# Performance work log

Hardware: AMD Instinct MI355X
Metric: run time of the kernel (lower is better)

## Reference

```python
import jax, jax.numpy as jnp
import numpy as np

B, N, F_IN = 512, 128, 133
NHID, NHEADS, HID = 64, 8, 512
FP_DIM, FP2, TASKS = 1489, 512, 12
ALPHA = 0.2
NEG_BIG = -9e15


def _lin_init(key, fan_in, fan_out):
    return jax.random.normal(key, (fan_in, fan_out), jnp.float32) / np.sqrt(fan_in)


def setup_inputs() -> dict:
    key = jax.random.key(0)
    ks = jax.random.split(key, 24)
    inp = {
        'h': jax.random.normal(ks[0], (B, N, F_IN), jnp.float32),
        'adj': jax.random.randint(ks[1], (B, N, N), 0, 2, jnp.int32),
        'edge_feat': jax.random.uniform(ks[2], (B, N, N), jnp.float32),
        'fp': jax.random.uniform(ks[3], (B, FP_DIM), jnp.float32),
        # multi-head GAT layer params (a split as [a1; a2; a_edge])
        'W_heads': jax.random.normal(ks[4], (NHEADS, F_IN, NHID), jnp.float32) / np.sqrt(F_IN),
        'a1_heads': jax.random.normal(ks[5], (NHEADS, NHID), jnp.float32) / np.sqrt(NHID),
        'a2_heads': jax.random.normal(ks[6], (NHEADS, NHID), jnp.float32) / np.sqrt(NHID),
        'ae_heads': jax.random.normal(ks[7], (NHEADS,), jnp.float32) * 0.1,
        # output GAT layer
        'W_out': jax.random.normal(ks[8], (NHID * NHEADS, HID), jnp.float32) / np.sqrt(NHID * NHEADS),
        'a1_out': jax.random.normal(ks[9], (HID,), jnp.float32) / np.sqrt(HID),
        'a2_out': jax.random.normal(ks[10], (HID,), jnp.float32) / np.sqrt(HID),
        'ae_out': jax.random.normal(ks[11], ()) * 0.1,
        # FPN
        'fc1_w': _lin_init(ks[12], FP_DIM, FP2), 'fc1_b': jnp.zeros((FP2,), jnp.float32),
        'fc2_w': _lin_init(ks[13], FP2, HID), 'fc2_b': jnp.zeros((HID,), jnp.float32),
        # cross-attention fusion
        'q_w': _lin_init(ks[14], HID, HID), 'q_b': jnp.zeros((HID,), jnp.float32),
        'k_w': _lin_init(ks[15], HID, HID), 'k_b': jnp.zeros((HID,), jnp.float32),
        'v_w': _lin_init(ks[16], HID, HID), 'v_b': jnp.zeros((HID,), jnp.float32),
        'o_w': _lin_init(ks[17], HID, HID), 'o_b': jnp.zeros((HID,), jnp.float32),
        # FFN head
        'ffn1_w': _lin_init(ks[18], HID, HID), 'ffn1_b': jnp.zeros((HID,), jnp.float32),
        'ffn2_w': _lin_init(ks[19], HID, TASKS), 'ffn2_b': jnp.zeros((TASKS,), jnp.float32),
    }
    return inp


def _leaky(x):
    return jnp.where(x >= 0, x, ALPHA * x)


def _fpgnn_forward(h, adj, edge_feat, fp,
                   W_heads, a1_heads, a2_heads, ae_heads,
                   W_out, a1_out, a2_out, ae_out,
                   fc1_w, fc1_b, fc2_w, fc2_b,
                   q_w, q_b, k_w, k_b, v_w, v_b, o_w, o_b,
                   ffn1_w, ffn1_b, ffn2_w, ffn2_b):
    mask = adj > 0  # [B,N,N]
    # --- multi-head GAT layers (concat=True) ---
    Wh = jnp.einsum('bnf,hfd->bhnd', h, W_heads)            # [B,H,N,D]
    s1 = jnp.einsum('bhnd,hd->bhn', Wh, a1_heads)
    s2 = jnp.einsum('bhnd,hd->bhn', Wh, a2_heads)
    # e[b,h,i,j] = leaky(Wh_i.a1 + Wh_j.a2 + edge_ij*ae)  (exact decomposition of
    # the original concat([Wh_i, Wh_j, edge_ij]) @ a)
    e = _leaky(s1[:, :, :, None] + s2[:, :, None, :]
               + edge_feat[:, None, :, :] * ae_heads[None, :, None, None])
    att = jnp.where(mask[:, None], e, NEG_BIG)
    att = jax.nn.softmax(att, axis=-1)                       # softmax over dim=1 of [N,N]
    hp = jnp.einsum('bhij,bhjd->bhid', att, Wh)
    x = jax.nn.elu(hp)                                       # concat=True -> ELU
    x = jnp.transpose(x, (0, 2, 1, 3)).reshape(B, N, NHEADS * NHID)
    # --- output GAT layer (concat=False) ---
    Wx = x @ W_out                                           # [B,N,HID]
    t1 = Wx @ a1_out                                         # [B,N]
    t2 = Wx @ a2_out
    e2 = _leaky(t1[:, :, None] + t2[:, None, :] + edge_feat * ae_out)
    att2 = jnp.where(mask, e2, NEG_BIG)
    att2 = jax.nn.softmax(att2, axis=-1)
    hp2 = jnp.einsum('bij,bjd->bid', att2, Wx)
    gat_nodes = jax.nn.elu(hp2)                              # F.elu in GATOne
    gat_out = gat_nodes.mean(axis=1)                         # molecule readout [B,HID]
    # --- FPN ---
    fpn_out = jax.nn.relu(fp @ fc1_w + fc1_b) @ fc2_w + fc2_b  # [B,HID]
    # --- cross-attention fusion ---
    q = gat_out @ q_w + q_b
    k = fpn_out @ k_w + k_b
    v = fpn_out @ v_w + v_b
    score = jnp.sum(q * k, axis=-1, keepdims=True) / np.sqrt(HID)  # [B,1]
    weight = jax.nn.softmax(score[:, :, None], axis=-1)[:, :, 0]    # softmax over size-1 dim -> ones
    fused = q + weight * v
    fused = jax.nn.relu(fused @ o_w + o_b)
    # --- FFN head (dropout p=0, eval) ---
    out = jax.nn.relu(fused @ ffn1_w + ffn1_b) @ ffn2_w + ffn2_b
    return out


def reference(h, adj, edge_feat, fp,
              W_heads, a1_heads, a2_heads, ae_heads,
              W_out, a1_out, a2_out, ae_out,
              fc1_w, fc1_b, fc2_w, fc2_b,
              q_w, q_b, k_w, k_b, v_w, v_b, o_w, o_b,
              ffn1_w, ffn1_b, ffn2_w, ffn2_b):
    return _fpgnn_forward(h, adj, edge_feat, fp,
                          W_heads, a1_heads, a2_heads, ae_heads,
                          W_out, a1_out, a2_out, ae_out,
                          fc1_w, fc1_b, fc2_w, fc2_b,
                          q_w, q_b, k_w, k_b, v_w, v_b, o_w, o_b,
                          ffn1_w, ffn1_b, ffn2_w, ffn2_b)
```

## Files before the change

### kernel.cpp

```cpp
#include <hip/hip_runtime.h>
#include <hip/hip_bf16.h>


#define ALPHA_LK 0.2f
#define KP1 192
#define KPF 1536
#define MINF_BF16 0xFF80u

typedef unsigned short ushort_t;
typedef __attribute__((ext_vector_type(8))) short bfrag;
typedef __attribute__((ext_vector_type(4))) float ffrag;

__device__ __forceinline__ float b2f(ushort_t u) {
  return __uint_as_float(((unsigned)u) << 16);
}
__device__ __forceinline__ ushort_t f2b(float f) {
  unsigned u = __float_as_uint(f);
  unsigned r = (u + 0x7fffu + ((u >> 16) & 1u)) >> 16;
  return (ushort_t)r;
}
__device__ __forceinline__ float elu1(float v) {
  return v > 0.f ? v : __expf(v) - 1.f;
}
__device__ __forceinline__ void unpack8(uint4 u, ushort_t* e) {
  e[0] = u.x & 0xffff; e[1] = u.x >> 16;
  e[2] = u.y & 0xffff; e[3] = u.y >> 16;
  e[4] = u.z & 0xffff; e[5] = u.z >> 16;
  e[6] = u.w & 0xffff; e[7] = u.w >> 16;
}
__device__ __forceinline__ uint4 pack8(const ushort_t* o) {
  uint4 u;
  u.x = o[0] | ((unsigned)o[1] << 16);
  u.y = o[2] | ((unsigned)o[3] << 16);
  u.z = o[4] | ((unsigned)o[5] << 16);
  u.w = o[6] | ((unsigned)o[7] << 16);
  return u;
}

__device__ __forceinline__ void gll16(const void* g, void* l) {
  __builtin_amdgcn_global_load_lds(
      (const __attribute__((address_space(1))) unsigned int*)(unsigned long long)g,
      (__attribute__((address_space(3))) unsigned int*)(unsigned long long)l,
      16, 0, 0);
}

__global__ __launch_bounds__(256) void repack_h(const float* __restrict__ h,
                                                ushort_t* __restrict__ hb) {
  int o = blockIdx.x * 256 + threadIdx.x;
  int row = o / 48, c4 = (o - row * 48) * 4;
  const float* hr = h + (size_t)row * 133;
  ushort4 v;
  v.x = (c4 + 0 < 133) ? f2b(hr[c4 + 0]) : (ushort_t)0;
  v.y = (c4 + 1 < 133) ? f2b(hr[c4 + 1]) : (ushort_t)0;
  v.z = (c4 + 2 < 133) ? f2b(hr[c4 + 2]) : (ushort_t)0;
  v.w = (c4 + 3 < 133) ? f2b(hr[c4 + 3]) : (ushort_t)0;
  *(ushort4*)&hb[(size_t)row * KP1 + c4] = v;
}

__global__ __launch_bounds__(256) void repack_fp(const float* __restrict__ fp,
                                                 ushort_t* __restrict__ fpb) {
  int o = blockIdx.x * 256 + threadIdx.x;
  int row = o / 384, c4 = (o - row * 384) * 4;
  const float* fr = fp + (size_t)row * 1489;
  ushort4 v;
  v.x = (c4 + 0 < 1489) ? f2b(fr[c4 + 0]) : (ushort_t)0;
  v.y = (c4 + 1 < 1489) ? f2b(fr[c4 + 1]) : (ushort_t)0;
  v.z = (c4 + 2 < 1489) ? f2b(fr[c4 + 2]) : (ushort_t)0;
  v.w = (c4 + 3 < 1489) ? f2b(fr[c4 + 3]) : (ushort_t)0;
  *(ushort4*)&fpb[(size_t)row * KPF + c4] = v;
}

__global__ __launch_bounds__(256) void repack_w2t(const float* __restrict__ Whd,
                                                  ushort_t* __restrict__ W2t) {
  int o = blockIdx.x * 256 + threadIdx.x;
  if (o >= 512 * 48) return;
  int col = o / 48, c4 = (o - col * 48) * 4;
  int hh = col >> 6, d = col & 63;
  ushort4 v;
  v.x = (c4 + 0 < 133) ? f2b(Whd[(hh * 133 + c4 + 0) * 64 + d]) : (ushort_t)0;
  v.y = (c4 + 1 < 133) ? f2b(Whd[(hh * 133 + c4 + 1) * 64 + d]) : (ushort_t)0;
  v.z = (c4 + 2 < 133) ? f2b(Whd[(hh * 133 + c4 + 2) * 64 + d]) : (ushort_t)0;
  v.w = (c4 + 3 < 133) ? f2b(Whd[(hh * 133 + c4 + 3) * 64 + d]) : (ushort_t)0;
  *(ushort4*)&W2t[(size_t)col * KP1 + c4] = v;
}

__global__ __launch_bounds__(256) void repack_t(const float* __restrict__ W,
                                                ushort_t* __restrict__ Wt,
                                                int K, int N, int Kpad) {
  int kp4 = Kpad >> 2;
  int o = blockIdx.x * 256 + threadIdx.x;
  if (o >= N * kp4) return;
  int col = o / kp4, k4 = (o - col * kp4) * 4;
  ushort4 v;
  v.x = (k4 + 0 < K) ? f2b(W[(size_t)(k4 + 0) * N + col]) : (ushort_t)0;
  v.y = (k4 + 1 < K) ? f2b(W[(size_t)(k4 + 1) * N + col]) : (ushort_t)0;
  v.z = (k4 + 2 < K) ? f2b(W[(size_t)(k4 + 2) * N + col]) : (ushort_t)0;
  v.w = (k4 + 3 < K) ? f2b(W[(size_t)(k4 + 3) * N + col]) : (ushort_t)0;
  *(ushort4*)&Wt[(size_t)col * Kpad + k4] = v;
}

__global__ __launch_bounds__(256) void repack_t7(
    const float* __restrict__ w0, const float* __restrict__ w1,
    const float* __restrict__ w2, const float* __restrict__ w3,
    const float* __restrict__ w4, const float* __restrict__ w5,
    const float* __restrict__ qb, const float* __restrict__ vb,
    ushort_t* __restrict__ d0, ushort_t* __restrict__ d1,
    ushort_t* __restrict__ d2, ushort_t* __restrict__ d3,
    ushort_t* __restrict__ d4, ushort_t* __restrict__ d5,
    float* __restrict__ qvb) {
  int y = blockIdx.y;
  int o = blockIdx.x * 256 + threadIdx.x;
  if (y == 6) {
    if (o < 512) qvb[o] = qb[o] + vb[o];
    return;
  }
  const float* W = y == 0 ? w0 : y == 1 ? w1 : y == 2 ? w2
                 : y == 3 ? w3 : y == 4 ? w4 : w5;
  ushort_t* Wt = y == 0 ? d0 : y == 1 ? d1 : y == 2 ? d2
               : y == 3 ? d3 : y == 4 ? d4 : d5;
  int col = o >> 7, k4 = (o & 127) * 4;
  ushort4 v;
  v.x = f2b(W[(size_t)(k4 + 0) * 512 + col]);
  v.y = f2b(W[(size_t)(k4 + 1) * 512 + col]);
  v.z = f2b(W[(size_t)(k4 + 2) * 512 + col]);
  v.w = f2b(W[(size_t)(k4 + 3) * 512 + col]);
  *(ushort4*)&Wt[(size_t)col * 512 + k4] = v;
}

__global__ __launch_bounds__(256) void repack_em(const float* __restrict__ edge,
                                                 const int* __restrict__ adj,
                                                 ushort_t* __restrict__ em) {
  size_t o = ((size_t)blockIdx.x * 256 + threadIdx.x) * 4;
  float4 e = *(const float4*)&edge[o];
  int4 a = *(const int4*)&adj[o];
  ushort4 v;
  v.x = a.x > 0 ? f2b(e.x) : (ushort_t)MINF_BF16;
  v.y = a.y > 0 ? f2b(e.y) : (ushort_t)MINF_BF16;
  v.z = a.z > 0 ? f2b(e.z) : (ushort_t)MINF_BF16;
  v.w = a.w > 0 ? f2b(e.w) : (ushort_t)MINF_BF16;
  *(ushort4*)&em[o] = v;
}

__global__ __launch_bounds__(256) void wa12_kernel(
    const float* __restrict__ W, const float* __restrict__ a1,
    const float* __restrict__ a2, float* __restrict__ wa1,
    float* __restrict__ wa2) {
  int wv = threadIdx.x >> 6, lane = threadIdx.x & 63;
  int k = blockIdx.x * 4 + wv;
  const float* wr = W + (size_t)k * 512;
  float p1 = 0.f, p2 = 0.f;
#pragma unroll
  for (int i = 0; i < 8; ++i) {
    float v = wr[lane + i * 64];
    p1 += v * a1[lane + i * 64];
    p2 += v * a2[lane + i * 64];
  }
#pragma unroll
  for (int off = 32; off; off >>= 1) {
    p1 += __shfl_down(p1, off);
    p2 += __shfl_down(p2, off);
  }
  if (lane == 0) { wa1[k] = p1; wa2[k] = p2; }
}

__global__ __launch_bounds__(256) void t12x_kernel(
    const ushort_t* __restrict__ xb, const float* __restrict__ wa1,
    const float* __restrict__ wa2, float* __restrict__ t1o,
    float* __restrict__ t2o, int base) {
  int wv = threadIdx.x >> 6, lane = threadIdx.x & 63;
  int row = blockIdx.x * 4 + wv;
  const ushort_t* xr = xb + (size_t)row * 512;
  ushort4 u0 = *(const ushort4*)&xr[lane * 8];
  ushort4 u1 = *(const ushort4*)&xr[lane * 8 + 4];
  float xv[8] = {b2f(u0.x), b2f(u0.y), b2f(u0.z), b2f(u0.w),
                 b2f(u1.x), b2f(u1.y), b2f(u1.z), b2f(u1.w)};
  float p1 = 0.f, p2 = 0.f;
#pragma unroll
  for (int i = 0; i < 8; ++i) {
    p1 += xv[i] * wa1[lane * 8 + i];
    p2 += xv[i] * wa2[lane * 8 + i];
  }
#pragma unroll
  for (int off = 32; off; off >>= 1) {
    p1 += __shfl_down(p1, off);
    p2 += __shfl_down(p2, off);
  }
  if (lane == 0) {
    t1o[base * 128 + row] = p1;
    t2o[base * 128 + row] = p2;
  }
}

__global__ __launch_bounds__(256) void att2_kernel(
    const ushort_t* __restrict__ em, const float* __restrict__ t1,
    const float* __restrict__ t2, const float* __restrict__ aeo,
    ushort_t* __restrict__ awg, float* __restrict__ sinvg, int base) {
  __shared__ float t2s[128];
  const int bl = blockIdx.x, bg = base + bl;
  const int t = threadIdx.x;
  if (t < 128) t2s[t] = t2[(size_t)bg * 128 + t];
  __syncthreads();
  const int row = t >> 1, half = t & 1;
  const float ae = aeo[0];
  const float rt1 = t1[(size_t)bg * 128 + row];
  const ushort_t* emr = em + (size_t)bg * 16384 + row * 128 + half * 64;
  ushort_t* awr = awg + (size_t)bl * 16384 + row * 128 + half * 64;
  float s = 0.f;
#pragma unroll
  for (int v = 0; v < 8; ++v) {
    ushort_t eu[8], ou[8];
    unpack8(*(const uint4*)&emr[v * 8], eu);
#pragma unroll
    for (int k = 0; k < 8; ++k) {
      float e = rt1 + t2s[half * 64 + v * 8 + k] + b2f(eu[k]) * ae;
      e = e >= 0.f ? e : ALPHA_LK * e;
      float pexp = (eu[k] != MINF_BF16) ? __expf(e) : 0.f;
      ou[k] = f2b(pexp);
      s += b2f(ou[k]);
    }
    *(uint4*)&awr[v * 8] = pack8(ou);
  }
  s += __shfl_xor(s, 1);
  if (!half) sinvg[(size_t)bl * 128 + row] = 1.f / fmaxf(s, 1e-30f);
}

__global__ __launch_bounds__(256) void fused_gat1(
    const ushort_t* __restrict__ hb, const ushort_t* __restrict__ W2t,
    const ushort_t* __restrict__ edgeM, const float* __restrict__ a1h,
    const float* __restrict__ a2h, const float* __restrict__ ae,
    ushort_t* __restrict__ x, int base) {
  __shared__ union {
    struct { ushort_t As[128][64]; ushort_t Bs[64][64]; } g;
    ushort_t WS[64][136];
  } u;
  __shared__ float ss1[128], ss2[128];
  const int id = blockIdx.x;
  const int hh = (id >> 3) & 7;
  const int bl = ((id >> 6) << 3) | (id & 7);
  const int bg = base + bl;
  const int t = threadIdx.x;
  const int lane = t & 63, w = t >> 6;
  const int l16 = lane & 15, quad = lane >> 4;
  const int w8 = w * 8, sr8 = (t >> 3) & 7;
  const int csw = ((t & 7) ^ sr8) << 3;

  const ushort_t* gA = hb + (size_t)(bl * 128 + w8 + sr8) * KP1 + csw;
  const ushort_t* gB = W2t + (size_t)(hh * 64 + w8 + sr8) * KP1 + csw;
  ffrag acc[2][4];
#pragma unroll
  for (int mi = 0; mi < 2; ++mi)
#pragma unroll
    for (int ni = 0; ni < 4; ++ni) acc[mi][ni] = {0.f, 0.f, 0.f, 0.f};
  for (int k0 = 0; k0 < KP1; k0 += 64) {
    __syncthreads();
#pragma unroll
    for (int p = 0; p < 4; ++p)
      gll16(gA + (size_t)(p * 32) * KP1 + k0, &u.g.As[p * 32 + w8][0]);
#pragma unroll
    for (int p = 0; p < 2; ++p)
      gll16(gB + (size_t)(p * 32) * KP1 + k0, &u.g.Bs[p * 32 + w8][0]);
    __syncthreads();
#pragma unroll
    for (int ks = 0; ks < 2; ++ks) {
      const int cs = ((ks * 4 + quad) ^ (l16 & 7)) << 3;
      bfrag af[2], bf[4];
#pragma unroll
      for (int mi = 0; mi < 2; ++mi)
        af[mi] = *(const bfrag*)&u.g.As[w * 32 + mi * 16 + l16][cs];
#pragma unroll
      for (int ni = 0; ni < 4; ++ni)
        bf[ni] = *(const bfrag*)&u.g.Bs[ni * 16 + l16][cs];
#pragma unroll
      for (int mi = 0; mi < 2; ++mi)
#pragma unroll
        for (int ni = 0; ni < 4; ++ni)
          acc[mi][ni] = __builtin_amdgcn_mfma_f32_16x16x32_bf16(
              af[mi], bf[ni], acc[mi][ni], 0, 0, 0);
    }
  }
  __syncthreads();

#pragma unroll
  for (int mi = 0; mi < 2; ++mi)
#pragma unroll
    for (int ni = 0; ni < 4; ++ni) {
      int col = ni * 16 + l16;
      int rowb = w * 32 + mi * 16 + quad * 4;
      ushort4 v;
      v.x = f2b(acc[mi][ni][0]);
      v.y = f2b(acc[mi][ni][1]);
      v.z = f2b(acc[mi][ni][2]);
      v.w = f2b(acc[mi][ni][3]);
      *(ushort4*)&u.WS[col][rowb] = v;
    }
  __syncthreads();

  uint4 ereg[2][4];
  {
    const ushort_t* em = edgeM + (size_t)bg * 16384;
#pragma unroll
    for (int mi = 0; mi < 2; ++mi) {
      int row = w * 32 + mi * 16 + l16;
#pragma unroll
      for (int ks = 0; ks < 4; ++ks)
        ereg[mi][ks] = *(const uint4*)&em[row * 128 + ks * 32 + quad * 8];
    }
  }
  {
    int n = t & 127;
    const float* av = (t < 128) ? a1h : a2h;
    float p = 0.f;
#pragma unroll 8
    for (int d = 0; d < 64; ++d) p += b2f(u.WS[d][n]) * av[hh * 64 + d];
    if (t < 128) ss1[n] = p; else ss2[n] = p;
  }
  __syncthreads();

  const float aeh = ae[hh];
  float rs1[2];
  rs1[0] = ss1[w * 32 + l16];
  rs1[1] = ss1[w * 32 + 16 + l16];
  uint4 aw[2][4];
  float rsum[2];
#pragma unroll
  for (int mi = 0; mi < 2; ++mi) {
    rsum[mi] = 0.f;
#pragma unroll
    for (int ks = 0; ks < 4; ++ks) {
      ushort_t eu[8], ou[8];
      unpack8(ereg[mi][ks], eu);
#pragma unroll
      for (int k = 0; k < 8; ++k) {
        float e = rs1[mi] + ss2[ks * 32 + quad * 8 + k] + b2f(eu[k]) * aeh;
        e = e >= 0.f ? e : ALPHA_LK * e;
        float pexp = (eu[k] != MINF_BF16) ? __expf(e) : 0.f;
        ou[k] = f2b(pexp);
        rsum[mi] += b2f(ou[k]);
      }
      aw[mi][ks] = pack8(ou);
    }
    rsum[mi] += __shfl_xor(rsum[mi], 16);
    rsum[mi] += __shfl_xor(rsum[mi], 32);
  }
  float sinv0 = 1.f / fmaxf(rsum[0], 1e-30f);
  float sinv1 = 1.f / fmaxf(rsum[1], 1e-30f);

  ffrag acc2[2][4];
#pragma unroll
  for (int mi = 0; mi < 2; ++mi)
#pragma unroll
    for (int ni = 0; ni < 4; ++ni) acc2[mi][ni] = {0.f, 0.f, 0.f, 0.f};
#pragma unroll
  for (int ks = 0; ks < 4; ++ks) {
    bfrag bfr[4];
#pragma unroll
    for (int ni = 0; ni < 4; ++ni)
      bfr[ni] = *(const bfrag*)&u.WS[ni * 16 + l16][ks * 32 + quad * 8];
#pragma unroll
    for (int mi = 0; mi < 2; ++mi) {
      bfrag afr;
      __builtin_memcpy(&afr, &aw[mi][ks], 16);
#pragma unroll
      for (int ni = 0; ni < 4; ++ni)
        acc2[mi][ni] = __builtin_amdgcn_mfma_f32_16x16x32_bf16(
            afr, bfr[ni], acc2[mi][ni], 0, 0, 0);
    }
  }
  float sv[2][4];
#pragma unroll
  for (int r = 0; r < 4; ++r) {
    sv[0][r] = __shfl(sinv0, quad * 4 + r);
    sv[1][r] = __shfl(sinv1, quad * 4 + r);
  }
#pragma unroll
  for (int mi = 0; mi < 2; ++mi)
#pragma unroll
    for (int ni = 0; ni < 4; ++ni)
#pragma unroll
      for (int r = 0; r < 4; ++r) {
        int rl = w * 32 + mi * 16 + quad * 4 + r;
        x[(size_t)(bl * 128 + rl) * 512 + hh * 64 + ni * 16 + l16] =
            f2b(elu1(acc2[mi][ni][r] * sv[mi][r]));
      }
}

__global__ __launch_bounds__(256) void fused_gat2(
    const ushort_t* __restrict__ xb, const ushort_t* __restrict__ Wot,
    const ushort_t* __restrict__ awg, const float* __restrict__ sinvg,
    ushort_t* __restrict__ gatb, int base) {
  __shared__ union {
    struct { ushort_t As[128][64]; ushort_t Bs[128][64]; } g;
    ushort_t WS[128][136];
  } u;
  __shared__ float ps[4][64];
  const int id = blockIdx.x;
  const int sp2 = (id >> 3) & 3;
  const int bl = ((id >> 5) << 3) | (id & 7);
  const int bg = base + bl;
  const int t = threadIdx.x;
  const int lane = t & 63, w = t >> 6;
  const int wm = w >> 1, wn = w & 1;
  const int l16 = lane & 15, quad = lane >> 4;
  const int w8 = w * 8, sr8 = (t >> 3) & 7;
  const int csw = ((t & 7) ^ sr8) << 3;

  const ushort_t* gA = xb + (size_t)(bl * 128 + w8 + sr8) * 512 + csw;
  const ushort_t* gB = Wot + (size_t)(sp2 * 128 + w8 + sr8) * 512 + csw;
  ffrag acc[4][4];
#pragma unroll
  for (int mi = 0; mi < 4; ++mi)
#pragma unroll
    for (int ni = 0; ni < 4; ++ni) acc[mi][ni] = {0.f, 0.f, 0.f, 0.f};
  for (int k0 = 0; k0 < 512; k0 += 64) {
    __syncthreads();
#pragma unroll
    for (int p = 0; p < 4; ++p) {
      gll16(gA + (size_t)(p * 32) * 512 + k0, &u.g.As[p * 32 + w8][0]);
      gll16(gB + (size_t)(p * 32) * 512 + k0, &u.g.Bs[p * 32 + w8][0]);
    }
    __syncthreads();
#pragma unroll
    for (int ks = 0; ks < 2; ++ks) {
      const int cs = ((ks * 4 + quad) ^ (l16 & 7)) << 3;
      bfrag af[4], bf[4];
#pragma unroll
      for (int i = 0; i < 4; ++i) {
        af[i] = *(const bfrag*)&u.g.As[wm * 64 + i * 16 + l16][cs];
        bf[i] = *(const bfrag*)&u.g.Bs[wn * 64 + i * 16 + l16][cs];
      }
#pragma unroll
      for (int mi = 0; mi < 4; ++mi)
#pragma unroll
        for (int ni = 0; ni < 4; ++ni)
          acc[mi][ni] = __builtin_amdgcn_mfma_f32_16x16x32_bf16(
              af[mi], bf[ni], acc[mi][ni], 0, 0, 0);
    }
  }
  __syncthreads();

#pragma unroll
  for (int mi = 0; mi < 4; ++mi)
#pragma unroll
    for (int ni = 0; ni < 4; ++ni) {
      int col = wn * 64 + ni * 16 + l16;
      int rowb = wm * 64 + mi * 16 + quad * 4;
      ushort4 v;
      v.x = f2b(acc[mi][ni][0]);
      v.y = f2b(acc[mi][ni][1]);
      v.z = f2b(acc[mi][ni][2]);
      v.w = f2b(acc[mi][ni][3]);
      *(ushort4*)&u.WS[col][rowb] = v;
    }
  __syncthreads();

  uint4 awf[2][4];
  float sv[2][4];
  {
    const ushort_t* ap = awg + (size_t)bl * 16384;
#pragma unroll
    for (int mi = 0; mi < 2; ++mi) {
      int row = w * 32 + mi * 16 + l16;
#pragma unroll
      for (int ks = 0; ks < 4; ++ks)
        awf[mi][ks] = *(const uint4*)&ap[row * 128 + ks * 32 + quad * 8];
      float si = sinvg[(size_t)bl * 128 + row];
#pragma unroll
      for (int r = 0; r < 4; ++r) sv[mi][r] = __shfl(si, quad * 4 + r);
    }
  }

  for (int s0 = 0; s0 < 2; ++s0) {
    ffrag acc2[2][4];
#pragma unroll
    for (int mi = 0; mi < 2; ++mi)
#pragma unroll
      for (int ni = 0; ni < 4; ++ni) acc2[mi][ni] = {0.f, 0.f, 0.f, 0.f};
#pragma unroll
    for (int ks = 0; ks < 4; ++ks) {
      bfrag bfr[4];
#pragma unroll
      for (int ni = 0; ni < 4; ++ni)
        bfr[ni] = *(const bfrag*)&u.WS[s0 * 64 + ni * 16 + l16][ks * 32 + quad * 8];
#pragma unroll
      for (int mi = 0; mi < 2; ++mi) {
        bfrag afr;
        __builtin_memcpy(&afr, &awf[mi][ks], 16);
#pragma unroll
        for (int ni = 0; ni < 4; ++ni)
          acc2[mi][ni] = __builtin_amdgcn_mfma_f32_16x16x32_bf16(
              afr, bfr[ni], acc2[mi][ni], 0, 0, 0);
      }
    }
    __syncthreads();
#pragma unroll
    for (int ni = 0; ni < 4; ++ni) {
      float s = 0.f;
#pragma unroll
      for (int mi = 0; mi < 2; ++mi)
#pragma unroll
        for (int r = 0; r < 4; ++r) s += elu1(acc2[mi][ni][r] * sv[mi][r]);
      s += __shfl_xor(s, 16);
      s += __shfl_xor(s, 32);
      if (quad == 0) ps[w][ni * 16 + l16] = s;
    }
    __syncthreads();
    if (t < 64) {
      float s = ps[0][t] + ps[1][t] + ps[2][t] + ps[3][t];
      gatb[(size_t)bg * 512 + sp2 * 128 + s0 * 64 + t] = f2b(s * (1.f / 128.f));
    }
  }
}

__device__ __forceinline__ void tail_kloop(
    const ushort_t* __restrict__ A, const ushort_t* __restrict__ Bt,
    int K, int ld, ushort_t (*As)[64], ushort_t (*Bs)[64],
    ffrag (*acc)[4], int row0, int col0, int t) {
  const int lane = t & 63, w = t >> 6;
  const int wm = w >> 1, wn = w & 1;
  const int l16 = lane & 15, quad = lane >> 4;
  const int w8 = w * 8, sr8 = (t >> 3) & 7;
  const int csw = ((t & 7) ^ sr8) << 3;
  const ushort_t* gA = A + (size_t)(row0 + w8 + sr8) * ld + csw;
  const ushort_t* gB = Bt + (size_t)(col0 + w8 + sr8) * ld + csw;
  for (int k0 = 0; k0 < K; k0 += 64) {
    __syncthreads();
#pragma unroll
    for (int p = 0; p < 4; ++p) {
      gll16(gA + (size_t)(p * 32) * ld + k0, &As[p * 32 + w8][0]);
      gll16(gB + (size_t)(p * 32) * ld + k0, &Bs[p * 32 + w8][0]);
    }
    __syncthreads();
#pragma unroll
    for (int ks = 0; ks < 2; ++ks) {
      const int cs = ((ks * 4 + quad) ^ (l16 & 7)) << 3;
      bfrag af[4], bf[4];
#pragma unroll
      for (int i = 0; i < 4; ++i) {
        af[i] = *(const bfrag*)&As[wm * 64 + i * 16 + l16][cs];
        bf[i] = *(const bfrag*)&Bs[wn * 64 + i * 16 + l16][cs];
      }
#pragma unroll
      for (int mi = 0; mi < 4; ++mi)
#pragma unroll
        for (int ni = 0; ni < 4; ++ni)
          acc[mi][ni] = __builtin_amdgcn_mfma_f32_16x16x32_bf16(
              af[mi], bf[ni], acc[mi][ni], 0, 0, 0);
    }
  }
}

template <int DUAL, int RELU>
__global__ __launch_bounds__(256) void gemm_tail(
    const ushort_t* __restrict__ A1, const ushort_t* __restrict__ Bt1,
    int K1, int ld1,
    const ushort_t* __restrict__ A2, const ushort_t* __restrict__ Bt2,
    const float* __restrict__ bias, ushort_t* __restrict__ C) {
  __shared__ ushort_t As[128][64];
  __shared__ ushort_t Bs[128][64];
  const int t = threadIdx.x;
  const int lane = t & 63, w = t >> 6;
  const int wm = w >> 1, wn = w & 1;
  const int l16 = lane & 15, quad = lane >> 4;
  const int row0 = blockIdx.y * 128, col0 = blockIdx.x * 128;

  ffrag acc[4][4];
#pragma unroll
  for (int mi = 0; mi < 4; ++mi)
#pragma unroll
    for (int ni = 0; ni < 4; ++ni) acc[mi][ni] = {0.f, 0.f, 0.f, 0.f};

  tail_kloop(A1, Bt1, K1, ld1, As, Bs, acc, row0, col0, t);
  if (DUAL) tail_kloop(A2, Bt2, 512, 512, As, Bs, acc, row0, col0, t);

#pragma unroll
  for (int mi = 0; mi < 4; ++mi)
#pragma unroll
    for (int ni = 0; ni < 4; ++ni) {
      int col = col0 + wn * 64 + ni * 16 + l16;
      float bb = bias[col];
#pragma unroll
      for (int r = 0; r < 4; ++r) {
        int row = row0 + wm * 64 + mi * 16 + quad * 4 + r;
        float v = acc[mi][ni][r] + bb;
        if (RELU) v = fmaxf(v, 0.f);
        C[(size_t)row * 512 + col] = f2b(v);
      }
    }
}

__global__ __launch_bounds__(256) void ffn2_kernel(
    const ushort_t* __restrict__ f5, const float* __restrict__ W,
    const float* __restrict__ b, float* __restrict__ out) {
  int wv = threadIdx.x >> 6, lane = threadIdx.x & 63;
  int row = blockIdx.x * 4 + wv;
  const ushort_t* fr = f5 + (size_t)row * 512;
  float v[8];
  ushort4 u0 = *(const ushort4*)&fr[lane * 8];
  ushort4 u1 = *(const ushort4*)&fr[lane * 8 + 4];
  v[0] = b2f(u0.x); v[1] = b2f(u0.y); v[2] = b2f(u0.z); v[3] = b2f(u0.w);
  v[4] = b2f(u1.x); v[5] = b2f(u1.y); v[6] = b2f(u1.z); v[7] = b2f(u1.w);
#pragma unroll
  for (int j = 0; j < 12; ++j) {
    float s = 0.f;
#pragma unroll
    for (int i = 0; i < 8; ++i) s += v[i] * W[(size_t)(lane * 8 + i) * 12 + j];
#pragma unroll
    for (int off = 32; off; off >>= 1) s += __shfl_down(s, off);
    if (lane == 0) out[(size_t)row * 12 + j] = s + b[j];
  }
}

extern "C" void kernel_launch(void* const* d_in, const int* in_sizes, int n_in,
                              void* d_out, int out_size, void* d_ws, size_t ws_size,
                              hipStream_t stream) {
  const float* h        = (const float*)d_in[0];
  const int*   adj      = (const int*)d_in[1];
  const float* edge     = (const float*)d_in[2];
  const float* fp       = (const float*)d_in[3];
  const float* W_heads  = (const float*)d_in[4];
  const float* a1_heads = (const float*)d_in[5];
  const float* a2_heads = (const float*)d_in[6];
  const float* ae_heads = (const float*)d_in[7];
  const float* W_out  = (const float*)d_in[8];
  const float* a1_out = (const float*)d_in[9];
  const float* a2_out = (const float*)d_in[10];
  const float* ae_out = (const float*)d_in[11];
  const float* fc1_w = (const float*)d_in[12];
  const float* fc1_b = (const float*)d_in[13];
  const float* fc2_w = (const float*)d_in[14];
  const float* fc2_b = (const float*)d_in[15];
  const float* q_w = (const float*)d_in[16];
  const float* q_b = (const float*)d_in[17];
  const float* v_w = (const float*)d_in[20];
  const float* v_b = (const float*)d_in[21];
  const float* o_w = (const float*)d_in[22];
  const float* o_b = (const float*)d_in[23];
  const float* ffn1_w = (const float*)d_in[24];
  const float* ffn1_b = (const float*)d_in[25];
  const float* ffn2_w = (const float*)d_in[26];
  const float* ffn2_b = (const float*)d_in[27];
  float* out = (float*)d_out;

  const size_t hb_bytes = (size_t)65536 * KP1 * 2;
  const size_t em_bytes = (size_t)512 * 16384 * 2;
  const size_t tail_bytes =
      (size_t)512 * KPF * 2 * 2 + (size_t)512 * 512 * 2 * 12 + 2048;
  const size_t fixed_bytes = hb_bytes + em_bytes + (size_t)512 * KP1 * 2 +
                             (size_t)2 * 65536 * 4 + tail_bytes + 16384;
  int C = 32;
  for (int cand = 512; cand >= 32; cand >>= 1) {
    size_t need = (size_t)cand * (131072 + 32768 + 512) + fixed_bytes;
    if (need <= ws_size) { C = cand; break; }
  }
  const int M = C * 128;

  char* p = (char*)d_ws;
  ushort_t* xb  = (ushort_t*)p; p += (size_t)C * 65536 * 2;
  ushort_t* awg = (ushort_t*)p; p += (size_t)C * 16384 * 2;
  float* sinv   = (float*)p;    p += (size_t)C * 128 * 4;
  ushort_t* hb  = (ushort_t*)p; p += hb_bytes;
  ushort_t* em  = (ushort_t*)p; p += em_bytes;
  ushort_t* W2t = (ushort_t*)p; p += (size_t)512 * KP1 * 2;
  float* t1 = (float*)p; p += 65536 * 4;
  float* t2 = (float*)p; p += 65536 * 4;
  ushort_t* fpb  = (ushort_t*)p; p += (size_t)512 * KPF * 2;
  ushort_t* fc1t = (ushort_t*)p; p += (size_t)512 * KPF * 2;
  ushort_t* Wot  = (ushort_t*)p; p += (size_t)512 * 512 * 2;
  ushort_t* fc2t = (ushort_t*)p; p += (size_t)512 * 512 * 2;
  ushort_t* qwt  = (ushort_t*)p; p += (size_t)512 * 512 * 2;
  ushort_t* vwt  = (ushort_t*)p; p += (size_t)512 * 512 * 2;
  ushort_t* owt  = (ushort_t*)p; p += (size_t)512 * 512 * 2;
  ushort_t* f1t  = (ushort_t*)p; p += (size_t)512 * 512 * 2;
  ushort_t* gatb = (ushort_t*)p; p += (size_t)512 * 512 * 2;
  ushort_t* fb1  = (ushort_t*)p; p += (size_t)512 * 512 * 2;
  ushort_t* fb2  = (ushort_t*)p; p += (size_t)512 * 512 * 2;
  ushort_t* fb3  = (ushort_t*)p; p += (size_t)512 * 512 * 2;
  ushort_t* fb4  = (ushort_t*)p; p += (size_t)512 * 512 * 2;
  ushort_t* fb5  = (ushort_t*)p; p += (size_t)512 * 512 * 2;
  float* qvb = (float*)p; p += 2048;
  float* wa1 = (float*)p; p += 2048;
  float* wa2 = (float*)p; p += 2048;

  repack_h<<<12288, 256, 0, stream>>>(h, hb);
  repack_em<<<8192, 256, 0, stream>>>(edge, adj, em);
  repack_w2t<<<96, 256, 0, stream>>>(W_heads, W2t);
  repack_fp<<<768, 256, 0, stream>>>(fp, fpb);
  repack_t<<<768, 256, 0, stream>>>(fc1_w, fc1t, 1489, 512, KPF);
  repack_t7<<<dim3(256, 7), 256, 0, stream>>>(
      W_out, fc2_w, q_w, v_w, o_w, ffn1_w, q_b, v_b,
      Wot, fc2t, qwt, vwt, owt, f1t, qvb);
  wa12_kernel<<<128, 256, 0, stream>>>(W_out, a1_out, a2_out, wa1, wa2);

  for (int base = 0; base < 512; base += C) {
    fused_gat1<<<8 * C, 256, 0, stream>>>(
        hb + (size_t)base * 128 * KP1, W2t, em, a1_heads, a2_heads,
        ae_heads, xb, base);
    t12x_kernel<<<M / 4, 256, 0, stream>>>(xb, wa1, wa2, t1, t2, base);
    att2_kernel<<<C, 256, 0, stream>>>(em, t1, t2, ae_out, awg, sinv, base);
    fused_gat2<<<4 * C, 256, 0, stream>>>(xb, Wot, awg, sinv, gatb, base);
  }

  gemm_tail<0, 1><<<dim3(4, 4), 256, 0, stream>>>(
      fpb, fc1t, KPF, KPF, nullptr, nullptr, fc1_b, fb1);
  gemm_tail<0, 0><<<dim3(4, 4), 256, 0, stream>>>(
      fb1, fc2t, 512, 512, nullptr, nullptr, fc2_b, fb2);
  gemm_tail<1, 0><<<dim3(4, 4), 256, 0, stream>>>(
      gatb, qwt, 512, 512, fb2, vwt, qvb, fb3);
  gemm_tail<0, 1><<<dim3(4, 4), 256, 0, stream>>>(
      fb3, owt, 512, 512, nullptr, nullptr, o_b, fb4);
  gemm_tail<0, 1><<<dim3(4, 4), 256, 0, stream>>>(
      fb4, f1t, 512, 512, nullptr, nullptr, ffn1_b, fb5);
  ffn2_kernel<<<128, 256, 0, stream>>>(fb5, ffn2_w, ffn2_b, out);
}
```

Measured before the change: 460.3 us.

## Use packed bf16 converts, exp2 softmax, MFMA row sums, and split att2 blocks

Replaces the scalar bf16 rounding with the hardware v_cvt_pk_bf16_f32 packed convert in every epilogue. Prescales the attention logits by log2(e) so the softmax can use the native exp2 instruction, and replaces the bit-shuffle unpacking with direct float reinterpretation. In fused_gat1, the softmax row sums come from an extra MFMA against a ones vector instead of shuffle reductions. att2 now launches twice as many blocks, each thread handling a quarter row. The aim is to cut VALU work in the elementwise phases; rounding and behaviour are meant to stay equivalent.

```diff
diff --git a/kernel.cpp b/kernel.cpp
--- a/kernel.cpp
+++ b/kernel.cpp
@@ -3,6 +3,7 @@
 
 
 #define ALPHA_LK 0.2f
+#define LOG2E 1.44269504f
 #define KP1 192
 #define KPF 1536
 #define MINF_BF16 0xFF80u
@@ -19,22 +20,25 @@
   unsigned r = (u + 0x7fffu + ((u >> 16) & 1u)) >> 16;
   return (ushort_t)r;
 }
+__device__ __forceinline__ unsigned cvt_pk(float lo, float hi) {
+  unsigned r;
+  asm("v_cvt_pk_bf16_f32 %0, %1, %2" : "=v"(r) : "v"(lo), "v"(hi));
+  return r;
+}
+__device__ __forceinline__ float frcp(float x) {
+  float r;
+  asm("v_rcp_f32 %0, %1" : "=v"(r) : "v"(x));
+  return r;
+}
+__device__ __forceinline__ float fexp2(float x) {
+#if __has_builtin(__builtin_amdgcn_exp2f)
+  return __builtin_amdgcn_exp2f(x);
+#else
+  return exp2f(x);
+#endif
+}
 __device__ __forceinline__ float elu1(float v) {
   return v > 0.f ? v : __expf(v) - 1.f;
-}
-__device__ __forceinline__ void unpack8(uint4 u, ushort_t* e) {
-  e[0] = u.x & 0xffff; e[1] = u.x >> 16;
-  e[2] = u.y & 0xffff; e[3] = u.y >> 16;
-  e[4] = u.z & 0xffff; e[5] = u.z >> 16;
-  e[6] = u.w & 0xffff; e[7] = u.w >> 16;
-}
-__device__ __forceinline__ uint4 pack8(const ushort_t* o) {
-  uint4 u;
-  u.x = o[0] | ((unsigned)o[1] << 16);
-  u.y = o[2] | ((unsigned)o[3] << 16);
-  u.z = o[4] | ((unsigned)o[5] << 16);
-  u.w = o[6] | ((unsigned)o[7] << 16);
-  return u;
 }
 
 __device__ __forceinline__ void gll16(const void* g, void* l) {
@@ -196,32 +200,41 @@
     const float* __restrict__ t2, const float* __restrict__ aeo,
     ushort_t* __restrict__ awg, float* __restrict__ sinvg, int base) {
   __shared__ float t2s[128];
-  const int bl = blockIdx.x, bg = base + bl;
+  const int bl = blockIdx.x >> 1, bg = base + bl;
+  const int rb = (blockIdx.x & 1) * 64;
   const int t = threadIdx.x;
-  if (t < 128) t2s[t] = t2[(size_t)bg * 128 + t];
+  if (t < 128) t2s[t] = t2[(size_t)bg * 128 + t] * LOG2E;
   __syncthreads();
-  const int row = t >> 1, half = t & 1;
-  const float ae = aeo[0];
-  const float rt1 = t1[(size_t)bg * 128 + row];
-  const ushort_t* emr = em + (size_t)bg * 16384 + row * 128 + half * 64;
-  ushort_t* awr = awg + (size_t)bl * 16384 + row * 128 + half * 64;
+  const int row = rb + (t >> 2), qtr = t & 3;
+  const float ae2 = aeo[0] * LOG2E;
+  const float rt1 = t1[(size_t)bg * 128 + row] * LOG2E;
+  const ushort_t* emr = em + (size_t)bg * 16384 + row * 128 + qtr * 32;
+  ushort_t* awr = awg + (size_t)bl * 16384 + row * 128 + qtr * 32;
   float s = 0.f;
 #pragma unroll
-  for (int v = 0; v < 8; ++v) {
-    ushort_t eu[8], ou[8];
-    unpack8(*(const uint4*)&emr[v * 8], eu);
-#pragma unroll
-    for (int k = 0; k < 8; ++k) {
-      float e = rt1 + t2s[half * 64 + v * 8 + k] + b2f(eu[k]) * ae;
-      e = e >= 0.f ? e : ALPHA_LK * e;
-      float pexp = (eu[k] != MINF_BF16) ? __expf(e) : 0.f;
-      ou[k] = f2b(pexp);
-      s += b2f(ou[k]);
-    }
-    *(uint4*)&awr[v * 8] = pack8(ou);
+  for (int v = 0; v < 4; ++v) {
+    uint4 eu = *(const uint4*)&emr[v * 8];
+    const unsigned uu[4] = {eu.x, eu.y, eu.z, eu.w};
+    unsigned po[4];
+#pragma unroll
+    for (int pr = 0; pr < 4; ++pr) {
+      float elo = __uint_as_float(uu[pr] << 16);
+      float ehi = __uint_as_float(uu[pr] & 0xffff0000u);
+      float e0 = fmaf(elo, ae2, rt1 + t2s[qtr * 32 + v * 8 + pr * 2]);
+      float e1 = fmaf(ehi, ae2, rt1 + t2s[qtr * 32 + v * 8 + pr * 2 + 1]);
+      e0 = fmaxf(e0, ALPHA_LK * e0);
+      e1 = fmaxf(e1, ALPHA_LK * e1);
+      float p0 = (elo != -INFINITY) ? fexp2(e0) : 0.f;
+      float p1 = (ehi != -INFINITY) ? fexp2(e1) : 0.f;
+      unsigned q = cvt_pk(p0, p1);
+      po[pr] = q;
+      s += __uint_as_float(q << 16) + __uint_as_float(q & 0xffff0000u);
+    }
+    *(uint4*)&awr[v * 8] = make_uint4(po[0], po[1], po[2], po[3]);
   }
   s += __shfl_xor(s, 1);
-  if (!half) sinvg[(size_t)bl * 128 + row] = 1.f / fmaxf(s, 1e-30f);
+  s += __shfl_xor(s, 2);
+  if (qtr == 0) sinvg[(size_t)bl * 128 + row] = 1.f / fmaxf(s, 1e-30f);
 }
 
 __global__ __launch_bounds__(256) void fused_gat1(
@@ -286,12 +299,10 @@
     for (int ni = 0; ni < 4; ++ni) {
       int col = ni * 16 + l16;
       int rowb = w * 32 + mi * 16 + quad * 4;
-      ushort4 v;
-      v.x = f2b(acc[mi][ni][0]);
-      v.y = f2b(acc[mi][ni][1]);
-      v.z = f2b(acc[mi][ni][2]);
-      v.w = f2b(acc[mi][ni][3]);
-      *(ushort4*)&u.WS[col][rowb] = v;
+      uint2 pv;
+      pv.x = cvt_pk(acc[mi][ni][0], acc[mi][ni][1]);
+      pv.y = cvt_pk(acc[mi][ni][2], acc[mi][ni][3]);
+      *(uint2*)&u.WS[col][rowb] = pv;
     }
   __syncthreads();
 
@@ -312,44 +323,54 @@
     float p = 0.f;
 #pragma unroll 8
     for (int d = 0; d < 64; ++d) p += b2f(u.WS[d][n]) * av[hh * 64 + d];
+    p *= LOG2E;
     if (t < 128) ss1[n] = p; else ss2[n] = p;
   }
   __syncthreads();
 
-  const float aeh = ae[hh];
+  const float aeh2 = ae[hh] * LOG2E;
   float rs1[2];
   rs1[0] = ss1[w * 32 + l16];
   rs1[1] = ss1[w * 32 + 16 + l16];
   uint4 aw[2][4];
-  float rsum[2];
 #pragma unroll
   for (int mi = 0; mi < 2; ++mi) {
-    rsum[mi] = 0.f;
 #pragma unroll
     for (int ks = 0; ks < 4; ++ks) {
-      ushort_t eu[8], ou[8];
-      unpack8(ereg[mi][ks], eu);
-#pragma unroll
-      for (int k = 0; k < 8; ++k) {
-        float e = rs1[mi] + ss2[ks * 32 + quad * 8 + k] + b2f(eu[k]) * aeh;
-        e = e >= 0.f ? e : ALPHA_LK * e;
-        float pexp = (eu[k] != MINF_BF16) ? __expf(e) : 0.f;
-        ou[k] = f2b(pexp);
-        rsum[mi] += b2f(ou[k]);
+      float s2v[8];
+      *(float4*)&s2v[0] = *(const float4*)&ss2[ks * 32 + quad * 8];
+      *(float4*)&s2v[4] = *(const float4*)&ss2[ks * 32 + quad * 8 + 4];
+      const unsigned uu[4] = {ereg[mi][ks].x, ereg[mi][ks].y,
+                              ereg[mi][ks].z, ereg[mi][ks].w};
+      unsigned po[4];
+#pragma unroll
+      for (int pr = 0; pr < 4; ++pr) {
+        float elo = __uint_as_float(uu[pr] << 16);
+        float ehi = __uint_as_float(uu[pr] & 0xffff0000u);
+        float e0 = fmaf(elo, aeh2, rs1[mi] + s2v[pr * 2]);
+        float e1 = fmaf(ehi, aeh2, rs1[mi] + s2v[pr * 2 + 1]);
+        e0 = fmaxf(e0, ALPHA_LK * e0);
+        e1 = fmaxf(e1, ALPHA_LK * e1);
+        float p0 = (elo != -INFINITY) ? fexp2(e0) : 0.f;
+        float p1 = (ehi != -INFINITY) ? fexp2(e1) : 0.f;
+        po[pr] = cvt_pk(p0, p1);
       }
-      aw[mi][ks] = pack8(ou);
-    }
-    rsum[mi] += __shfl_xor(rsum[mi], 16);
-    rsum[mi] += __shfl_xor(rsum[mi], 32);
-  }
-  float sinv0 = 1.f / fmaxf(rsum[0], 1e-30f);
-  float sinv1 = 1.f / fmaxf(rsum[1], 1e-30f);
+      aw[mi][ks] = make_uint4(po[0], po[1], po[2], po[3]);
+    }
+  }
+
+  bfrag bones;
+#pragma unroll
+  for (int i = 0; i < 8; ++i) bones[i] = (short)0x3F80;
 
   ffrag acc2[2][4];
-#pragma unroll
-  for (int mi = 0; mi < 2; ++mi)
+  ffrag accs[2];
+#pragma unroll
+  for (int mi = 0; mi < 2; ++mi) {
+    accs[mi] = {0.f, 0.f, 0.f, 0.f};
 #pragma unroll
     for (int ni = 0; ni < 4; ++ni) acc2[mi][ni] = {0.f, 0.f, 0.f, 0.f};
+  }
 #pragma unroll
   for (int ks = 0; ks < 4; ++ks) {
     bfrag bfr[4];
@@ -364,24 +385,33 @@
       for (int ni = 0; ni < 4; ++ni)
         acc2[mi][ni] = __builtin_amdgcn_mfma_f32_16x16x32_bf16(
             afr, bfr[ni], acc2[mi][ni], 0, 0, 0);
+      accs[mi] = __builtin_amdgcn_mfma_f32_16x16x32_bf16(
+          afr, bones, accs[mi], 0, 0, 0);
     }
   }
   float sv[2][4];
 #pragma unroll
-  for (int r = 0; r < 4; ++r) {
-    sv[0][r] = __shfl(sinv0, quad * 4 + r);
-    sv[1][r] = __shfl(sinv1, quad * 4 + r);
-  }
-#pragma unroll
   for (int mi = 0; mi < 2; ++mi)
 #pragma unroll
-    for (int ni = 0; ni < 4; ++ni)
-#pragma unroll
-      for (int r = 0; r < 4; ++r) {
-        int rl = w * 32 + mi * 16 + quad * 4 + r;
-        x[(size_t)(bl * 128 + rl) * 512 + hh * 64 + ni * 16 + l16] =
-            f2b(elu1(acc2[mi][ni][r] * sv[mi][r]));
-      }
+    for (int r = 0; r < 4; ++r)
+      sv[mi][r] = frcp(fmaxf(accs[mi][r], 1e-30f));
+
+#pragma unroll
+  for (int mi = 0; mi < 2; ++mi)
+#pragma unroll
+    for (int ni = 0; ni < 4; ++ni) {
+      float e0 = elu1(acc2[mi][ni][0] * sv[mi][0]);
+      float e1 = elu1(acc2[mi][ni][1] * sv[mi][1]);
+      float e2 = elu1(acc2[mi][ni][2] * sv[mi][2]);
+      float e3 = elu1(acc2[mi][ni][3] * sv[mi][3]);
+      unsigned p01 = cvt_pk(e0, e1), p23 = cvt_pk(e2, e3);
+      int rl = w * 32 + mi * 16 + quad * 4;
+      size_t bo = (size_t)(bl * 128 + rl) * 512 + hh * 64 + ni * 16 + l16;
+      x[bo] = (ushort_t)p01;
+      x[bo + 512] = (ushort_t)(p01 >> 16);
+      x[bo + 1024] = (ushort_t)p23;
+      x[bo + 1536] = (ushort_t)(p23 >> 16);
+    }
 }
 
 __global__ __launch_bounds__(256) void fused_gat2(
@@ -444,12 +474,10 @@
     for (int ni = 0; ni < 4; ++ni) {
       int col = wn * 64 + ni * 16 + l16;
       int rowb = wm * 64 + mi * 16 + quad * 4;
-      ushort4 v;
-      v.x = f2b(acc[mi][ni][0]);
-      v.y = f2b(acc[mi][ni][1]);
-      v.z = f2b(acc[mi][ni][2]);
-      v.w = f2b(acc[mi][ni][3]);
-      *(ushort4*)&u.WS[col][rowb] = v;
+      uint2 pv;
+      pv.x = cvt_pk(acc[mi][ni][0], acc[mi][ni][1]);
+      pv.y = cvt_pk(acc[mi][ni][2], acc[mi][ni][3]);
+      *(uint2*)&u.WS[col][rowb] = pv;
     }
   __syncthreads();
 
@@ -578,13 +606,19 @@
     for (int ni = 0; ni < 4; ++ni) {
       int col = col0 + wn * 64 + ni * 16 + l16;
       float bb = bias[col];
-#pragma unroll
-      for (int r = 0; r < 4; ++r) {
-        int row = row0 + wm * 64 + mi * 16 + quad * 4 + r;
-        float v = acc[mi][ni][r] + bb;
-        if (RELU) v = fmaxf(v, 0.f);
-        C[(size_t)row * 512 + col] = f2b(v);
+      float v0 = acc[mi][ni][0] + bb, v1 = acc[mi][ni][1] + bb;
+      float v2 = acc[mi][ni][2] + bb, v3 = acc[mi][ni][3] + bb;
+      if (RELU) {
+        v0 = fmaxf(v0, 0.f); v1 = fmaxf(v1, 0.f);
+        v2 = fmaxf(v2, 0.f); v3 = fmaxf(v3, 0.f);
       }
+      unsigned p01 = cvt_pk(v0, v1), p23 = cvt_pk(v2, v3);
+      int row = row0 + wm * 64 + mi * 16 + quad * 4;
+      size_t o = (size_t)row * 512 + col;
+      C[o] = (ushort_t)p01;
+      C[o + 512] = (ushort_t)(p01 >> 16);
+      C[o + 1024] = (ushort_t)p23;
+      C[o + 1536] = (ushort_t)(p23 >> 16);
     }
 }
 
@@ -696,7 +730,7 @@
         hb + (size_t)base * 128 * KP1, W2t, em, a1_heads, a2_heads,
         ae_heads, xb, base);
     t12x_kernel<<<M / 4, 256, 0, stream>>>(xb, wa1, wa2, t1, t2, base);
-    att2_kernel<<<C, 256, 0, stream>>>(em, t1, t2, ae_out, awg, sinv, base);
+    att2_kernel<<<2 * C, 256, 0, stream>>>(em, t1, t2, ae_out, awg, sinv, base);
     fused_gat2<<<4 * C, 256, 0, stream>>>(xb, Wot, awg, sinv, gatb, base);
   }
 
```

New measurement: 461.0 us. Within noise of the previous version (+0.1%).
